# Optimization experiments

Measured on AMD Instinct MI355X. Metric: run time of the kernel, lower is better.

## Reference

```python
import jax, jax.numpy as jnp
import numpy as np

NUM_GROUPS = 8
EPS = 1e-6

def group_norm(x, gamma, beta):
    # x: [B, C, L]
    B, C, L = x.shape
    g = x.reshape(B, NUM_GROUPS, (C // NUM_GROUPS) * L)
    mean = g.mean(axis=-1, keepdims=True)
    var = g.var(axis=-1, keepdims=True)
    g = (g - mean) * jax.lax.rsqrt(var + EPS)
    g = g.reshape(B, C, L)
    return g * gamma[None, :, None] + beta[None, :, None]

def conv1x1(h, w, b):
    # w: [O, C], b: [O]; h: [B, C, L]
    return jnp.einsum('oc,bcl->bol', w, h) + b[None, :, None]

def setup_inputs() -> dict:
    key = jax.random.key(0)
    ks = jax.random.split(key, 12)
    B, C, L = 8, 512, 2048
    s = 1.0 / np.sqrt(C)
    inp = {
        'x': jax.random.normal(ks[0], (B, C, L), dtype=jnp.float32),
        'gamma': jnp.ones((C,), jnp.float32),
        'beta': jnp.zeros((C,), jnp.float32),
        'wq': jax.random.uniform(ks[1], (C, C), jnp.float32, -s, s),
        'bq': jax.random.uniform(ks[2], (C,), jnp.float32, -s, s),
        'wk': jax.random.uniform(ks[3], (C, C), jnp.float32, -s, s),
        'bk': jax.random.uniform(ks[4], (C,), jnp.float32, -s, s),
        'wv': jax.random.uniform(ks[5], (C, C), jnp.float32, -s, s),
        'bv': jax.random.uniform(ks[6], (C,), jnp.float32, -s, s),
        'wo': jax.random.uniform(ks[7], (C, C), jnp.float32, -s, s),
        'bo': jax.random.uniform(ks[8], (C,), jnp.float32, -s, s),
    }
    return inp

def reference(x, gamma, beta, wq, bq, wk, bk, wv, bv, wo, bo):
    C = x.shape[1]
    h = group_norm(x, gamma, beta)
    q = conv1x1(h, wq, bq)  # [B, C, L]
    k = conv1x1(h, wk, bk)
    v = conv1x1(h, wv, bv)
    # scores: [B, Lq, Lk] = q^T k, scaled by C^-0.5
    w = jnp.einsum('bci,bcj->bij', q, k) * (C ** -0.5)
    w = jax.nn.softmax(w, axis=2)
    # h[b,c,i] = sum_j v[b,c,j] * w[b,i,j]
    h = jnp.einsum('bcj,bij->bci', v, w)
    h = conv1x1(h, wo, bo)
    return x + h
```

## Files before the change

### kernel.cpp

```cpp
#include <hip/hip_runtime.h>
#include <hip/hip_bf16.h>
#include <cstdio>

typedef __attribute__((ext_vector_type(8))) short short8;
typedef __attribute__((ext_vector_type(8))) unsigned short ushort8;
typedef __attribute__((ext_vector_type(4))) float f32x4;
typedef __attribute__((ext_vector_type(4))) unsigned short ushort4v;

__device__ inline unsigned short f2bf(float f){
    unsigned int u = __float_as_uint(f);
    unsigned int r = (u + 0x7fffu + ((u >> 16) & 1u)) >> 16;
    return (unsigned short)r;
}
__device__ inline float bf2f(unsigned short b){
    return __uint_as_float((unsigned int)b << 16);
}

__device__ inline void store1(float* p, float v){ *p = v; }
__device__ inline void store1(unsigned short* p, float v){ *p = f2bf(v); }

#define GLDS(gp, lp) __builtin_amdgcn_global_load_lds( \
    (const __attribute__((address_space(1))) void*)(gp), \
    (__attribute__((address_space(3))) void*)(lp), 16, 0, 0)

#define WAITV(N) asm volatile("s_waitcnt vmcnt(" #N ")" ::: "memory")

template<typename OutT, int EPI>
__global__ __launch_bounds__(512, 2)
void gemm256(const unsigned short* __restrict__ Ag,
             const unsigned short* __restrict__ Bg,
             OutT* __restrict__ Cg,
             int K, int lda, int ldb, int ldc,
             long sA, long sB, long sC,
             const float* __restrict__ bias,
             const float* __restrict__ resid, long sR,
             float scale)
{
    const int gx = gridDim.x, gy = gridDim.y;
    const int nwg  = gx * gy * (int)gridDim.z;
    const int orig = blockIdx.x + gx * (blockIdx.y + gy * blockIdx.z);
    const int cpx  = nwg >> 3;
    const int nid  = (orig & 7) * cpx + (orig >> 3);
    const int bx   = nid % gx;
    const int tmp  = nid / gx;
    const int by   = tmp % gy;
    const int bz   = tmp / gy;

    Ag += (long)bz * sA;
    Bg += (long)bz * sB;
    Cg += (long)bz * sC;
    const int m0 = by * 256;
    const int n0 = bx * 256;

    __shared__ unsigned short As[2][16384];
    __shared__ unsigned short Bs[2][16384];

    const int t    = threadIdx.x;
    const int wave = t >> 6;
    const int lane = t & 63;
    const int rg   = wave >> 2;
    const int cg   = wave & 3;
    const int wm   = rg * 128;
    const int wn   = cg * 64;
    const int lhi  = lane >> 4;
    const int llo  = lane & 15;

    f32x4 acc[4][8];
#pragma unroll
    for (int p = 0; p < 4; p++)
#pragma unroll
        for (int f = 0; f < 8; f++) acc[p][f] = (f32x4)(0.0f);

    const int s_rr = t >> 3, s_cb = t & 7;
    const int s_cs = s_cb ^ (s_rr & 7);
    auto stageA = [&](int bi, int k0, int j){
        GLDS(Ag + (long)(m0 + j * 64 + s_rr) * lda + k0 + s_cs * 8,
             &As[bi][j * 4096 + wave * 512]);
    };
    auto stageB = [&](int bi, int k0, int j){
        GLDS(Bg + (long)(n0 + j * 64 + s_rr) * ldb + k0 + s_cs * 8,
             &Bs[bi][j * 4096 + wave * 512]);
    };

    const int nt = K >> 6;
    stageB(0, 0, 0); stageB(0, 0, 1); stageB(0, 0, 2); stageB(0, 0, 3);
    stageA(0, 0, 0); stageA(0, 0, 2); stageA(0, 0, 1); stageA(0, 0, 3);
    WAITV(2);
    __builtin_amdgcn_s_barrier();
    __builtin_amdgcn_sched_barrier(0);

    int cur = 0;
    for (int kt = 0; kt < nt; kt++){
        const bool more = (kt + 1 < nt);
        const int nk0 = (kt + 1) << 6;
#pragma unroll
        for (int p = 0; p < 4; p++){
            const int h = p >> 1, cl = p & 1;
            short8 af[2][4], bf[2][2];
#pragma unroll
            for (int ks = 0; ks < 2; ks++){
#pragma unroll
                for (int mi = 0; mi < 4; mi++){
                    const int r  = wm + h * 64 + mi * 16 + llo;
                    const int pc = (ks * 4 + lhi) ^ (r & 7);
                    af[ks][mi] = *(const short8*)(&As[cur][r * 64 + pc * 8]);
                }
#pragma unroll
                for (int ni = 0; ni < 2; ni++){
                    const int r  = wn + cl * 32 + ni * 16 + llo;
                    const int pc = (ks * 4 + lhi) ^ (r & 7);
                    bf[ks][ni] = *(const short8*)(&Bs[cur][r * 64 + pc * 8]);
                }
            }
            __builtin_amdgcn_sched_barrier(0);
            if (more){
                if (p == 0){ stageB(cur ^ 1, nk0, 0); stageB(cur ^ 1, nk0, 1); }
                if (p == 1){ stageB(cur ^ 1, nk0, 2); stageB(cur ^ 1, nk0, 3); }
                if (p == 2){ stageA(cur ^ 1, nk0, 0); stageA(cur ^ 1, nk0, 2); }
                if (p == 3){ stageA(cur ^ 1, nk0, 1); stageA(cur ^ 1, nk0, 3); }
            }
            if (p == 1){ if (more) WAITV(4); else WAITV(0); }
            if (p == 3){ if (more) WAITV(2); }
            __builtin_amdgcn_s_barrier();
            __builtin_amdgcn_sched_barrier(0);
            __builtin_amdgcn_s_setprio(1);
#pragma unroll
            for (int ks = 0; ks < 2; ks++)
#pragma unroll
                for (int mi = 0; mi < 4; mi++)
#pragma unroll
                    for (int ni = 0; ni < 2; ni++)
                        acc[p][mi * 2 + ni] = __builtin_amdgcn_mfma_f32_16x16x32_bf16(
                            af[ks][mi], bf[ks][ni], acc[p][mi * 2 + ni], 0, 0, 0);
            __builtin_amdgcn_s_setprio(0);
            __builtin_amdgcn_s_barrier();
            __builtin_amdgcn_sched_barrier(0);
        }
        cur ^= 1;
    }

#pragma unroll
    for (int p = 0; p < 4; p++){
        const int h = p >> 1, cl = p & 1;
#pragma unroll
        for (int mi = 0; mi < 4; mi++){
#pragma unroll
            for (int ni = 0; ni < 2; ni++){
                const int n  = n0 + wn + cl * 32 + ni * 16 + llo;
                const int mb = m0 + wm + h * 64 + mi * 16 + lhi * 4;
                f32x4 v = acc[p][mi * 2 + ni];
#pragma unroll
                for (int j = 0; j < 4; j++){
                    const int m = mb + j;
                    float val = v[j] * scale;
                    if (EPI == 1) val += bias[n];
                    if (EPI == 2) val += bias[m];
                    if (EPI == 3) val += bias[m] + resid[(long)bz * sR + (long)m * ldc + n];
                    store1(&Cg[(long)m * ldc + n], val);
                }
            }
        }
    }
}

template<typename OutT, int EPI>
__global__ __launch_bounds__(256)
void gemm_nt(const unsigned short* __restrict__ Ag,
             const unsigned short* __restrict__ Bg,
             OutT* __restrict__ Cg,
             int K, int lda, int ldb, int ldc,
             long sA, long sB, long sC,
             const float* __restrict__ bias,
             const float* __restrict__ resid, long sR,
             float scale)
{
    const int gx = gridDim.x, gy = gridDim.y;
    const int nwg  = gx * gy * (int)gridDim.z;
    const int orig = blockIdx.x + gx * (blockIdx.y + gy * blockIdx.z);
    const int cpx  = nwg >> 3;
    const int nid  = (orig & 7) * cpx + (orig >> 3);
    const int bx   = nid % gx;
    const int tmp  = nid / gx;
    const int by   = tmp % gy;
    const int bz   = tmp / gy;

    Ag += (long)bz * sA;
    Bg += (long)bz * sB;
    Cg += (long)bz * sC;
    const int m0 = by * 128;
    const int n0 = bx * 128;

    __shared__ unsigned short As[2][128 * 64];
    __shared__ unsigned short Bs[2][128 * 64];

    const int t    = threadIdx.x;
    const int wave = t >> 6;
    const int lane = t & 63;
    const int wm   = (wave >> 1) << 6;
    const int wn   = (wave & 1) << 6;
    const int lhi  = lane >> 4;
    const int llo  = lane & 15;

    f32x4 acc[4][4];
#pragma unroll
    for (int i = 0; i < 4; i++)
#pragma unroll
        for (int j = 0; j < 4; j++) acc[i][j] = (f32x4)(0.0f);

    auto stage = [&](int bi, int k0){
#pragma unroll
        for (int i = 0; i < 4; i++){
            const int tt = i * 256 + t;
            const int r  = tt >> 3;
            const int cb = tt & 7;
            const int cs = cb ^ (r & 7);
            GLDS(Ag + (long)(m0 + r) * lda + k0 + cs * 8, &As[bi][i * 2048 + wave * 512]);
            GLDS(Bg + (long)(n0 + r) * ldb + k0 + cs * 8, &Bs[bi][i * 2048 + wave * 512]);
        }
    };

    const int nt = K >> 6;
    stage(0, 0);
    __syncthreads();

    int cur = 0;
    for (int kt = 0; kt < nt; kt++){
        if (kt + 1 < nt) stage(cur ^ 1, (kt + 1) << 6);
#pragma unroll
        for (int ksub = 0; ksub < 2; ksub++){
            short8 af[4], bf[4];
#pragma unroll
            for (int mi = 0; mi < 4; mi++){
                const int r  = wm + mi * 16 + llo;
                const int cs = (ksub * 4 + lhi) ^ (r & 7);
                af[mi] = *(const short8*)(&As[cur][r * 64 + cs * 8]);
            }
#pragma unroll
            for (int ni = 0; ni < 4; ni++){
                const int r  = wn + ni * 16 + llo;
                const int cs = (ksub * 4 + lhi) ^ (r & 7);
                bf[ni] = *(const short8*)(&Bs[cur][r * 64 + cs * 8]);
            }
#pragma unroll
            for (int mi = 0; mi < 4; mi++)
#pragma unroll
                for (int ni = 0; ni < 4; ni++)
                    acc[mi][ni] = __builtin_amdgcn_mfma_f32_16x16x32_bf16(
                        af[mi], bf[ni], acc[mi][ni], 0, 0, 0);
        }
        __syncthreads();
        cur ^= 1;
    }

#pragma unroll
    for (int mi = 0; mi < 4; mi++){
#pragma unroll
        for (int ni = 0; ni < 4; ni++){
            const int n  = n0 + wn + ni * 16 + llo;
            const int mb = m0 + wm + mi * 16 + lhi * 4;
            f32x4 v = acc[mi][ni];
#pragma unroll
            for (int j = 0; j < 4; j++){
                const int m = mb + j;
                float val = v[j] * scale;
                if (EPI == 1) val += bias[n];
                if (EPI == 2) val += bias[m];
                if (EPI == 3) val += bias[m] + resid[(long)bz * sR + (long)m * ldc + n];
                store1(&Cg[(long)m * ldc + n], val);
            }
        }
    }
}


__global__ void gn_partial(const float* __restrict__ x, float* __restrict__ part){
    const long base = (long)blockIdx.x * 8192;
    const float4* xp = (const float4*)(x + base);
    float s = 0.f, ss = 0.f;
    for (int i = threadIdx.x; i < 2048; i += 256){
        float4 v = xp[i];
        s  += (v.x + v.y) + (v.z + v.w);
        ss += (v.x * v.x + v.y * v.y) + (v.z * v.z + v.w * v.w);
    }
    for (int o = 32; o; o >>= 1){ s += __shfl_down(s, o); ss += __shfl_down(ss, o); }
    __shared__ float rs[4], rss[4];
    const int wave = threadIdx.x >> 6, lane = threadIdx.x & 63;
    if (lane == 0){ rs[wave] = s; rss[wave] = ss; }
    __syncthreads();
    if (threadIdx.x == 0){
        part[blockIdx.x * 2]     = (rs[0] + rs[1]) + (rs[2] + rs[3]);
        part[blockIdx.x * 2 + 1] = (rss[0] + rss[1]) + (rss[2] + rss[3]);
    }
}

__global__ void gn_final(const float* __restrict__ part, float* __restrict__ stats){
    const int bg = threadIdx.x;
    if (bg >= 64) return;
    float s = 0.f, ss = 0.f;
    for (int c = 0; c < 16; c++){
        s  += part[(bg * 16 + c) * 2];
        ss += part[(bg * 16 + c) * 2 + 1];
    }
    const float inv_n = 1.0f / 131072.0f;
    const float mean = s * inv_n;
    const float var  = ss * inv_n - mean * mean;
    stats[bg * 2]     = mean;
    stats[bg * 2 + 1] = rsqrtf(var + 1e-6f);
}

__global__ void norm_transpose(const float* __restrict__ x, const float* __restrict__ stats,
                               const float* __restrict__ gamma, const float* __restrict__ beta,
                               unsigned short* __restrict__ ht){
    const int b = blockIdx.z, c0 = blockIdx.y * 64, l0 = blockIdx.x * 64;
    const int bg = b * 8 + (c0 >> 6);
    const float mean = stats[bg * 2], rstd = stats[bg * 2 + 1];
    __shared__ unsigned short tile[64][66];
    const float* xb = x + (long)b * 1048576;
    const int t = threadIdx.x;
#pragma unroll
    for (int i = 0; i < 16; i++){
        const int idx = i * 256 + t;
        const int c = idx >> 6, l = idx & 63;
        float v = xb[(long)(c0 + c) * 2048 + l0 + l];
        v = (v - mean) * rstd * gamma[c0 + c] + beta[c0 + c];
        tile[l][c] = f2bf(v);
    }
    __syncthreads();
    unsigned short* htb = ht + (long)b * 1048576;
#pragma unroll
    for (int i = 0; i < 16; i++){
        const int idx = i * 256 + t;
        const int l = idx >> 6, c = idx & 63;
        htb[(long)(l0 + l) * 512 + c0 + c] = tile[l][c];
    }
}

__global__ void weights_to_bf16(const float4* __restrict__ wq, const float4* __restrict__ wk,
                                const float4* __restrict__ wv, const float4* __restrict__ wo,
                                ushort4v* __restrict__ out){
    const int i = blockIdx.x * 256 + threadIdx.x;
    const int w = i >> 16, off = i & 65535;
    const float4* src = (w == 0) ? wq : (w == 1) ? wk : (w == 2) ? wv : wo;
    float4 v = src[off];
    ushort4v o;
    o.x = f2bf(v.x); o.y = f2bf(v.y); o.z = f2bf(v.z); o.w = f2bf(v.w);
    out[i] = o;
}

__global__ void softmax_inplace(unsigned short* __restrict__ p){
    const long base = (long)blockIdx.x * 2048;
    ushort8* pp = (ushort8*)(p + base);
    const int t = threadIdx.x;
    ushort8 v = pp[t];
    float f[8];
#pragma unroll
    for (int j = 0; j < 8; j++) f[j] = bf2f(v[j]);
    float mx = f[0];
#pragma unroll
    for (int j = 1; j < 8; j++) mx = fmaxf(mx, f[j]);
    for (int o = 32; o; o >>= 1) mx = fmaxf(mx, __shfl_xor(mx, o));
    __shared__ float rmax[4], rsum[4];
    const int wave = t >> 6, lane = t & 63;
    if (lane == 0) rmax[wave] = mx;
    __syncthreads();
    mx = fmaxf(fmaxf(rmax[0], rmax[1]), fmaxf(rmax[2], rmax[3]));
    float sum = 0.f;
#pragma unroll
    for (int j = 0; j < 8; j++){ f[j] = __expf(f[j] - mx); sum += f[j]; }
    for (int o = 32; o; o >>= 1) sum += __shfl_xor(sum, o);
    if (lane == 0) rsum[wave] = sum;
    __syncthreads();
    sum = (rsum[0] + rsum[1]) + (rsum[2] + rsum[3]);
    const float inv = 1.0f / sum;
    ushort8 o8;
#pragma unroll
    for (int j = 0; j < 8; j++) o8[j] = f2bf(f[j] * inv);
    pp[t] = o8;
}

enum : long {
    OFF_WQ  = 0,
    OFF_WK  = 524288,
    OFF_WV  = 1048576,
    OFF_WO  = 1572864,
    OFF_HT  = 2097152,
    OFF_QT  = OFF_HT  + 16777216,
    OFF_KT  = OFF_QT  + 16777216,
    OFF_V   = OFF_KT  + 16777216,
    OFF_H2  = OFF_V   + 16777216,
    OFF_P   = OFF_H2  + 16777216,
    OFF_GNP = OFF_P   + 67108864,
    OFF_GNS = OFF_GNP + 8192,
    OFF_END = OFF_GNS + 512
};

extern "C" void kernel_launch(void* const* d_in, const int* in_sizes, int n_in,
                              void* d_out, int out_size, void* d_ws, size_t ws_size,
                              hipStream_t stream)
{
    const float* x     = (const float*)d_in[0];
    const float* gamma = (const float*)d_in[1];
    const float* beta  = (const float*)d_in[2];
    const float* wq    = (const float*)d_in[3];
    const float* bq    = (const float*)d_in[4];
    const float* wk    = (const float*)d_in[5];
    const float* bk    = (const float*)d_in[6];
    const float* wv    = (const float*)d_in[7];
    const float* bv    = (const float*)d_in[8];
    const float* wo    = (const float*)d_in[9];
    const float* bo    = (const float*)d_in[10];
    float* out = (float*)d_out;
    char* ws = (char*)d_ws;

    if (ws_size < (size_t)OFF_END){
        fprintf(stderr, "kernel_launch: ws too small (%zu < %ld)\n", ws_size, (long)OFF_END);
        return;
    }

    unsigned short* HT  = (unsigned short*)(ws + OFF_HT);
    unsigned short* QT  = (unsigned short*)(ws + OFF_QT);
    unsigned short* KT  = (unsigned short*)(ws + OFF_KT);
    unsigned short* V   = (unsigned short*)(ws + OFF_V);
    unsigned short* H2  = (unsigned short*)(ws + OFF_H2);
    unsigned short* P   = (unsigned short*)(ws + OFF_P);
    float*          GNP = (float*)(ws + OFF_GNP);
    float*          GNS = (float*)(ws + OFF_GNS);
    unsigned short* WQb = (unsigned short*)(ws + OFF_WQ);
    unsigned short* WKb = (unsigned short*)(ws + OFF_WK);
    unsigned short* WVb = (unsigned short*)(ws + OFF_WV);
    unsigned short* WOb = (unsigned short*)(ws + OFF_WO);

    const long LC = 1048576;
    const long LL = 4194304;

    weights_to_bf16<<<1024, 256, 0, stream>>>(
        (const float4*)wq, (const float4*)wk, (const float4*)wv, (const float4*)wo,
        (ushort4v*)(ws + OFF_WQ));

    gn_partial<<<1024, 256, 0, stream>>>(x, GNP);
    gn_final<<<1, 64, 0, stream>>>(GNP, GNS);
    norm_transpose<<<dim3(32, 8, 8), 256, 0, stream>>>(x, GNS, gamma, beta, HT);

    gemm_nt<unsigned short, 1><<<dim3(4, 16, 8), 256, 0, stream>>>(
        HT, WQb, QT, 512, 512, 512, 512, LC, 0, LC, bq, nullptr, 0, 1.0f);
    gemm_nt<unsigned short, 1><<<dim3(4, 16, 8), 256, 0, stream>>>(
        HT, WKb, KT, 512, 512, 512, 512, LC, 0, LC, bk, nullptr, 0, 1.0f);
    gemm_nt<unsigned short, 2><<<dim3(16, 4, 8), 256, 0, stream>>>(
        WVb, HT, V, 512, 512, 512, 2048, 0, LC, LC, bv, nullptr, 0, 1.0f);

    gemm256<unsigned short, 0><<<dim3(8, 8, 8), 512, 0, stream>>>(
        QT, KT, P, 512, 512, 512, 2048, LC, LC, LL, nullptr, nullptr, 0, 0.04419417382f);

    softmax_inplace<<<16384, 256, 0, stream>>>(P);

    gemm256<unsigned short, 0><<<dim3(2, 8, 8), 512, 0, stream>>>(
        P, V, H2, 2048, 2048, 2048, 512, LL, LC, LC, nullptr, nullptr, 0, 1.0f);

    gemm_nt<float, 3><<<dim3(16, 4, 8), 256, 0, stream>>>(
        WOb, H2, out, 512, 512, 512, 2048, 0, LC, LC, bo, x, LC, 1.0f);
}
```

Baseline: 309.0 us.

## Reuse A/B fragments across quadrants in gemm256 and switch PV GEMM to gemm_nt

The gemm256 main loop is restructured so that each k-tile loads A and B fragments once per half and reuses them across quadrants in a snake order (acc0, acc1, acc2, acc3). This cuts LDS reads from 4x(A+B) per tile down to roughly 2A+2B. The stage and wait schedule is re-laid to match, and the epilogue writes each quadrant in that order. Separately, the P·V GEMM (M=2048, N=512, K=2048, only 128 workgroups) now uses gemm_nt with a 4x16x8 grid, giving more workgroups, in exchange for a smaller tile and less reuse.

```diff
diff --git a/kernel.cpp b/kernel.cpp
--- a/kernel.cpp
+++ b/kernel.cpp
@@ -24,6 +24,16 @@
     (__attribute__((address_space(3))) void*)(lp), 16, 0, 0)
 
 #define WAITV(N) asm volatile("s_waitcnt vmcnt(" #N ")" ::: "memory")
+
+#define MFMA_Q(ACC, AF, BF) \
+    _Pragma("unroll") \
+    for (int ks = 0; ks < 2; ks++) \
+        _Pragma("unroll") \
+        for (int mi = 0; mi < 4; mi++) \
+            _Pragma("unroll") \
+            for (int ni = 0; ni < 2; ni++) \
+                ACC[mi * 2 + ni] = __builtin_amdgcn_mfma_f32_16x16x32_bf16( \
+                    AF[ks][mi], BF[ks][ni], ACC[mi * 2 + ni], 0, 0, 0);
 
 template<typename OutT, int EPI>
 __global__ __launch_bounds__(512, 2)
@@ -65,11 +75,12 @@
     const int lhi  = lane >> 4;
     const int llo  = lane & 15;
 
-    f32x4 acc[4][8];
-#pragma unroll
-    for (int p = 0; p < 4; p++)
-#pragma unroll
-        for (int f = 0; f < 8; f++) acc[p][f] = (f32x4)(0.0f);
+    f32x4 acc0[8], acc1[8], acc2[8], acc3[8];
+#pragma unroll
+    for (int f = 0; f < 8; f++){
+        acc0[f] = (f32x4)(0.0f); acc1[f] = (f32x4)(0.0f);
+        acc2[f] = (f32x4)(0.0f); acc3[f] = (f32x4)(0.0f);
+    }
 
     const int s_rr = t >> 3, s_cb = t & 7;
     const int s_cs = s_cb ^ (s_rr & 7);
@@ -93,62 +104,90 @@
     for (int kt = 0; kt < nt; kt++){
         const bool more = (kt + 1 < nt);
         const int nk0 = (kt + 1) << 6;
-#pragma unroll
-        for (int p = 0; p < 4; p++){
-            const int h = p >> 1, cl = p & 1;
-            short8 af[2][4], bf[2][2];
-#pragma unroll
-            for (int ks = 0; ks < 2; ks++){
-#pragma unroll
-                for (int mi = 0; mi < 4; mi++){
-                    const int r  = wm + h * 64 + mi * 16 + llo;
-                    const int pc = (ks * 4 + lhi) ^ (r & 7);
-                    af[ks][mi] = *(const short8*)(&As[cur][r * 64 + pc * 8]);
-                }
-#pragma unroll
-                for (int ni = 0; ni < 2; ni++){
-                    const int r  = wn + cl * 32 + ni * 16 + llo;
-                    const int pc = (ks * 4 + lhi) ^ (r & 7);
-                    bf[ks][ni] = *(const short8*)(&Bs[cur][r * 64 + pc * 8]);
-                }
-            }
-            __builtin_amdgcn_sched_barrier(0);
-            if (more){
-                if (p == 0){ stageB(cur ^ 1, nk0, 0); stageB(cur ^ 1, nk0, 1); }
-                if (p == 1){ stageB(cur ^ 1, nk0, 2); stageB(cur ^ 1, nk0, 3); }
-                if (p == 2){ stageA(cur ^ 1, nk0, 0); stageA(cur ^ 1, nk0, 2); }
-                if (p == 3){ stageA(cur ^ 1, nk0, 1); stageA(cur ^ 1, nk0, 3); }
-            }
-            if (p == 1){ if (more) WAITV(4); else WAITV(0); }
-            if (p == 3){ if (more) WAITV(2); }
-            __builtin_amdgcn_s_barrier();
-            __builtin_amdgcn_sched_barrier(0);
-            __builtin_amdgcn_s_setprio(1);
-#pragma unroll
-            for (int ks = 0; ks < 2; ks++)
-#pragma unroll
-                for (int mi = 0; mi < 4; mi++)
-#pragma unroll
-                    for (int ni = 0; ni < 2; ni++)
-                        acc[p][mi * 2 + ni] = __builtin_amdgcn_mfma_f32_16x16x32_bf16(
-                            af[ks][mi], bf[ks][ni], acc[p][mi * 2 + ni], 0, 0, 0);
-            __builtin_amdgcn_s_setprio(0);
-            __builtin_amdgcn_s_barrier();
-            __builtin_amdgcn_sched_barrier(0);
+        short8 af[2][4], bf0[2][2], bf1[2][2];
+
+#pragma unroll
+        for (int ks = 0; ks < 2; ks++){
+#pragma unroll
+            for (int mi = 0; mi < 4; mi++){
+                const int r  = wm + mi * 16 + llo;
+                const int pc = (ks * 4 + lhi) ^ (r & 7);
+                af[ks][mi] = *(const short8*)(&As[cur][r * 64 + pc * 8]);
+            }
+#pragma unroll
+            for (int ni = 0; ni < 2; ni++){
+                const int r  = wn + ni * 16 + llo;
+                const int pc = (ks * 4 + lhi) ^ (r & 7);
+                bf0[ks][ni] = *(const short8*)(&Bs[cur][r * 64 + pc * 8]);
+            }
         }
+        __builtin_amdgcn_sched_barrier(0);
+        if (more){ stageB(cur ^ 1, nk0, 0); stageB(cur ^ 1, nk0, 1); }
+        __builtin_amdgcn_s_barrier();
+        __builtin_amdgcn_sched_barrier(0);
+        __builtin_amdgcn_s_setprio(1);
+        MFMA_Q(acc0, af, bf0);
+        __builtin_amdgcn_s_setprio(0);
+        __builtin_amdgcn_s_barrier();
+        __builtin_amdgcn_sched_barrier(0);
+
+#pragma unroll
+        for (int ks = 0; ks < 2; ks++)
+#pragma unroll
+            for (int ni = 0; ni < 2; ni++){
+                const int r  = wn + 32 + ni * 16 + llo;
+                const int pc = (ks * 4 + lhi) ^ (r & 7);
+                bf1[ks][ni] = *(const short8*)(&Bs[cur][r * 64 + pc * 8]);
+            }
+        __builtin_amdgcn_sched_barrier(0);
+        if (more){ stageB(cur ^ 1, nk0, 2); stageB(cur ^ 1, nk0, 3); WAITV(4); }
+        else     { WAITV(0); }
+        __builtin_amdgcn_s_barrier();
+        __builtin_amdgcn_sched_barrier(0);
+        __builtin_amdgcn_s_setprio(1);
+        MFMA_Q(acc1, af, bf1);
+        __builtin_amdgcn_s_setprio(0);
+        __builtin_amdgcn_s_barrier();
+        __builtin_amdgcn_sched_barrier(0);
+
+#pragma unroll
+        for (int ks = 0; ks < 2; ks++)
+#pragma unroll
+            for (int mi = 0; mi < 4; mi++){
+                const int r  = wm + 64 + mi * 16 + llo;
+                const int pc = (ks * 4 + lhi) ^ (r & 7);
+                af[ks][mi] = *(const short8*)(&As[cur][r * 64 + pc * 8]);
+            }
+        __builtin_amdgcn_sched_barrier(0);
+        if (more){ stageA(cur ^ 1, nk0, 0); stageA(cur ^ 1, nk0, 2); }
+        __builtin_amdgcn_s_barrier();
+        __builtin_amdgcn_sched_barrier(0);
+        __builtin_amdgcn_s_setprio(1);
+        MFMA_Q(acc2, af, bf1);
+        __builtin_amdgcn_s_setprio(0);
+        __builtin_amdgcn_s_barrier();
+        __builtin_amdgcn_sched_barrier(0);
+
+        if (more){ stageA(cur ^ 1, nk0, 1); stageA(cur ^ 1, nk0, 3); WAITV(2); }
+        __builtin_amdgcn_s_barrier();
+        __builtin_amdgcn_sched_barrier(0);
+        __builtin_amdgcn_s_setprio(1);
+        MFMA_Q(acc3, af, bf0);
+        __builtin_amdgcn_s_setprio(0);
+        __builtin_amdgcn_s_barrier();
+        __builtin_amdgcn_sched_barrier(0);
+
         cur ^= 1;
     }
 
-#pragma unroll
-    for (int p = 0; p < 4; p++){
-        const int h = p >> 1, cl = p & 1;
+    auto epi = [&](f32x4 (&A)[8], int h, int cl){
 #pragma unroll
         for (int mi = 0; mi < 4; mi++){
 #pragma unroll
             for (int ni = 0; ni < 2; ni++){
                 const int n  = n0 + wn + cl * 32 + ni * 16 + llo;
                 const int mb = m0 + wm + h * 64 + mi * 16 + lhi * 4;
-                f32x4 v = acc[p][mi * 2 + ni];
+                f32x4 v = A[mi * 2 + ni];
 #pragma unroll
                 for (int j = 0; j < 4; j++){
                     const int m = mb + j;
@@ -160,7 +199,8 @@
                 }
             }
         }
-    }
+    };
+    epi(acc0, 0, 0); epi(acc1, 0, 1); epi(acc2, 1, 1); epi(acc3, 1, 0);
 }
 
 template<typename OutT, int EPI>
@@ -453,7 +493,7 @@
 
     softmax_inplace<<<16384, 256, 0, stream>>>(P);
 
-    gemm256<unsigned short, 0><<<dim3(2, 8, 8), 512, 0, stream>>>(
+    gemm_nt<unsigned short, 0><<<dim3(4, 16, 8), 256, 0, stream>>>(
         P, V, H2, 2048, 2048, 2048, 512, LL, LC, LC, nullptr, nullptr, 0, 1.0f);
 
     gemm_nt<float, 3><<<dim3(16, 4, 8), 256, 0, stream>>>(
```

After: 276.9 us. 10.4% less time.
